# Optimization experiments

Hardware: AMD Instinct MI355X
Metric: run time of the kernel (lower is better)

## Reference

```python
import jax, jax.numpy as jnp
import numpy as np

N = 32            # batch (age.shape[0])
N_SAMPLE = 8
S = N * N_SAMPLE  # posterior samples
T = 1024          # len_param
K = 64            # len_window
D = 4             # dim_target
P = 8             # dim_param
LOG2PI = float(np.log(2.0 * np.pi))


def _windows(x, axis, num, size):
    # torch.unfold equivalent, but window axis inserted right after `axis`
    idx = jnp.arange(num)[:, None] + jnp.arange(size)[None, :]
    return jnp.take(x, idx, axis=axis)


def _coeffs(a_pad):
    # a_pad: (2K-2, D, 1) -> AR weight matrix d: (K, K, D)
    # d[t, k] = prod(a[t-K+1+k+1 .. t]) with trailing 1 (reversed cumprod of windows)
    b = _windows(a_pad, 0, K, K - 1)                              # (K, K-1, D, 1)
    c = jnp.flip(jnp.cumprod(jnp.flip(b, 1), axis=1), 1)
    d = jnp.concatenate([c, jnp.ones_like(c[:, :1])], axis=1)      # (K, K, D, 1)
    return d[..., 0]                                               # (K, K, D)


def _window_param(z, d):
    # z: (S, K, D, P); d: (K, K, D) -> param: (S, K, D, P)
    z_pad = jnp.pad(z, ((0, 0), (K - 1, 0), (0, 0), (0, 0)))
    zwin = _windows(z_pad, 1, K, K)                                # (S, K, K, D, P)
    return jnp.einsum('stkdp,tkd->stdp', zwin, d)


def _forward(m, s_raw, a_raw, noise, dim_idx):
    mm = m[:, dim_idx]                         # (T, D, P)
    s = jax.nn.softplus(s_raw[:, dim_idx])     # scale_transform
    a = jax.nn.sigmoid(a_raw[:, dim_idx])      # (T-1, D, 1)
    # ---- first window ----
    a_pad = jnp.pad(a[:K - 1], ((K - 1, 0), (0, 0), (0, 0)))       # (2K-2, D, 1)
    mean = (1.0 - a_pad[K - 2:]) * mm[:K]                          # (K, D, P)
    sw = s[:K]
    z = mean + sw * noise[:, :K]                                   # rsample
    lp = -jnp.log(sw) - 0.5 * LOG2PI - 0.5 * ((z - mean) / sw) ** 2
    param = _window_param(z, _coeffs(a_pad))
    params, lps = [param], [lp]
    # ---- subsequent windows (sequential carry via param[:, -1]) ----
    for l in range(K, T, K):
        r = min(l + K, T)
        aw = a[l - 1:r - 1]                                        # (K, D, 1)
        mean = (1.0 - aw) * mm[l:r]
        sw = s[l:r]
        z = mean + sw * noise[:, l:r]
        lp = -jnp.log(sw) - 0.5 * LOG2PI - 0.5 * ((z - mean) / sw) ** 2
        a_pad = jnp.pad(aw[1:], ((K - 1, 0), (0, 0), (0, 0)))
        p = _window_param(z, _coeffs(a_pad))
        p = p + jnp.cumprod(aw, axis=0)[None] * param[:, -1][:, None]
        params.append(p)
        lps.append(lp)
        param = p
    return jnp.concatenate(params, axis=1), jnp.concatenate(lps, axis=1)


def setup_inputs() -> dict:
    key = jax.random.key(0)
    k = jax.random.split(key, 6)
    return {
        'y': jax.random.normal(k[0], (1, T, D), dtype=jnp.float32),
        'age': jax.random.uniform(k[1], (N,), dtype=jnp.float32),
        'm': 0.1 * jax.random.normal(k[2], (T, D, P), dtype=jnp.float32),
        's_raw': 0.1 * jax.random.normal(k[3], (T, D, P), dtype=jnp.float32) - 6.0,
        'a_raw': jax.random.normal(k[4], (T - 1, D, 1), dtype=jnp.float32),
        'noise': jax.random.normal(k[5], (S, T, D, P), dtype=jnp.float32),
        'cond_sample': jnp.zeros((S, D, P), dtype=jnp.float32),
        'dim_idx': jnp.arange(D, dtype=jnp.int32),
        'compute_log_prob': 1,
    }


def reference(y, age, m, s_raw, a_raw, noise, cond_sample, dim_idx, compute_log_prob):
    param, log_prob = _forward(m, s_raw, a_raw, noise, dim_idx)
    if compute_log_prob:
        return (param, log_prob)
    return param
```

## Files before the change

### kernel.cpp

```cpp
#include <hip/hip_runtime.h>
#include <hip/hip_bf16.h>

#define T_DIM 1024
#define D_DIM 4
#define P_DIM 8
#define S_DIM 256
#define DP 32
#define TDP (T_DIM * DP)
#define LOG2PI_F 1.8378770664093453f

__global__ __launch_bounds__(256) void build_tbl(
    const float* __restrict__ m,
    const float* __restrict__ s_raw,
    const float* __restrict__ a_raw,
    const int* __restrict__ dim_idx,
    float4* __restrict__ tbl)
{
    int idx = blockIdx.x * 256 + threadIdx.x;
    int t  = idx >> 5;
    int dp = idx & 31;
    int d  = dp >> 3;
    int p  = dp & 7;
    int di = dim_idx[d];

    float mm = m[(t * D_DIM + di) * P_DIM + p];
    float sr = s_raw[(t * D_DIM + di) * P_DIM + p];
    float sv = (sr > 20.0f) ? sr : log1pf(expf(sr));

    float A = 0.0f;
    if (t > 0) {
        float ar = a_raw[(t - 1) * D_DIM + di];
        A = 1.0f / (1.0f + expf(-ar));
    }
    float mean = (1.0f - A) * mm;
    float nls  = -logf(sv) - 0.5f * LOG2PI_F;

    tbl[idx] = make_float4(mean, sv, nls, A);
}

__global__ __launch_bounds__(256) void scan_kernel(
    const float* __restrict__ noise,
    const float4* __restrict__ tbl,
    float* __restrict__ param_out,
    float* __restrict__ lp_out)
{
    const int s   = blockIdx.x;
    const int tid = threadIdx.x;
    const int dp  = tid & 31;
    const int cj  = tid >> 5;

    __shared__ float sh_pl[8][32];
    __shared__ float sh_m[8][32];
    __shared__ float sh_ci[8][32];

    const size_t sbase = (size_t)s * TDP;

    float carry = 0.0f;

    float  na[8];
    float4 ca[8];
    {
        const int tb = (cj * 8) * DP + dp;
        #pragma unroll
        for (int k = 0; k < 8; ++k) {
            na[k] = noise[sbase + tb + k * DP];
            ca[k] = tbl[tb + k * DP];
        }
    }

    for (int tile = 0; tile < 16; ++tile) {
        float  nb[8];
        float4 cb[8];
        {
            const int tn  = (tile + 1 < 16) ? tile + 1 : 0;
            const int tb2 = (tn * 64 + cj * 8) * DP + dp;
            #pragma unroll
            for (int k = 0; k < 8; ++k) {
                nb[k] = noise[sbase + tb2 + k * DP];
                cb[k] = tbl[tb2 + k * DP];
            }
        }

        const int tb = (tile * 64 + cj * 8) * DP + dp;

        float pl[8], Mk[8];
        float rp = 0.0f, rm = 1.0f;
        #pragma unroll
        for (int k = 0; k < 8; ++k) {
            const float n = na[k];
            const float z = ca[k].x + ca[k].y * n;
            lp_out[sbase + tb + k * DP] = ca[k].z - 0.5f * n * n;
            rp = z + ca[k].w * rp;
            rm = rm * ca[k].w;
            pl[k] = rp;
            Mk[k] = rm;
        }

        sh_pl[cj][dp] = rp;
        sh_m[cj][dp]  = rm;
        __syncthreads();

        if (cj == 0) {
            float cr = carry;
            #pragma unroll
            for (int cc = 0; cc < 8; ++cc) {
                sh_ci[cc][dp] = cr;
                cr = sh_pl[cc][dp] + sh_m[cc][dp] * cr;
            }
            carry = cr;
        }
        __syncthreads();

        const float ci = sh_ci[cj][dp];
        #pragma unroll
        for (int k = 0; k < 8; ++k) {
            param_out[sbase + tb + k * DP] = pl[k] + Mk[k] * ci;
        }

        #pragma unroll
        for (int k = 0; k < 8; ++k) { na[k] = nb[k]; ca[k] = cb[k]; }
    }
}

extern "C" void kernel_launch(void* const* d_in, const int* in_sizes, int n_in,
                              void* d_out, int out_size, void* d_ws, size_t ws_size,
                              hipStream_t stream)
{
    const float* m      = (const float*)d_in[2];
    const float* s_raw  = (const float*)d_in[3];
    const float* a_raw  = (const float*)d_in[4];
    const float* noise  = (const float*)d_in[5];
    const int*   dimidx = (const int*)d_in[7];

    float4* tbl = (float4*)d_ws;

    float* param_out = (float*)d_out;
    float* lp_out    = param_out + (size_t)S_DIM * TDP;

    build_tbl<<<TDP / 256, 256, 0, stream>>>(m, s_raw, a_raw, dimidx, tbl);
    scan_kernel<<<S_DIM, 256, 0, stream>>>(noise, tbl, param_out, lp_out);
}
```

Measured before the change: 126.1 us.

## Scan whole sequence per block with 1024 threads, wave shuffles and SoA table

The scan kernel now uses 1024 threads per sample. Each thread handles 8 timesteps of 4 contiguous dp lanes using float4 loads and stores, which replaces the 16 serial tiles of the old kernel. The coefficient table moves from array-of-float4 to structure-of-arrays so the accesses vectorise. The cross-chunk carry combines a wave-level shuffle scan with one 16-step shared-memory pass, which removes the per-tile barriers and serial carry loop. In exchange, register pressure rises with 1024-thread blocks, and the explicit next-tile prefetch of the old kernel is gone.

Measured after the change: 129.7 us. +2.8%, slower.

```diff
diff --git a/kernel.cpp b/kernel.cpp
--- a/kernel.cpp
+++ b/kernel.cpp
@@ -1,5 +1,4 @@
 #include <hip/hip_runtime.h>
-#include <hip/hip_bf16.h>
 
 #define T_DIM 1024
 #define D_DIM 4
@@ -14,111 +13,132 @@
     const float* __restrict__ s_raw,
     const float* __restrict__ a_raw,
     const int* __restrict__ dim_idx,
-    float4* __restrict__ tbl)
+    float* __restrict__ tbl)
 {
     int idx = blockIdx.x * 256 + threadIdx.x;
-    int t  = idx >> 5;
-    int dp = idx & 31;
-    int d  = dp >> 3;
-    int p  = dp & 7;
+    int t = idx >> 5, dp = idx & 31, d = dp >> 3, p = dp & 7;
     int di = dim_idx[d];
 
     float mm = m[(t * D_DIM + di) * P_DIM + p];
     float sr = s_raw[(t * D_DIM + di) * P_DIM + p];
     float sv = (sr > 20.0f) ? sr : log1pf(expf(sr));
+    float A = 0.0f;
+    if (t > 0) A = 1.0f / (1.0f + expf(-a_raw[(t - 1) * D_DIM + di]));
 
-    float A = 0.0f;
-    if (t > 0) {
-        float ar = a_raw[(t - 1) * D_DIM + di];
-        A = 1.0f / (1.0f + expf(-ar));
-    }
-    float mean = (1.0f - A) * mm;
-    float nls  = -logf(sv) - 0.5f * LOG2PI_F;
-
-    tbl[idx] = make_float4(mean, sv, nls, A);
+    tbl[idx]           = (1.0f - A) * mm;
+    tbl[TDP + idx]     = sv;
+    tbl[2 * TDP + idx] = -logf(sv) - 0.5f * LOG2PI_F;
+    tbl[3 * TDP + idx] = A;
 }
 
-__global__ __launch_bounds__(256) void scan_kernel(
+__global__ __launch_bounds__(1024) void scan_kernel(
     const float* __restrict__ noise,
-    const float4* __restrict__ tbl,
+    const float* __restrict__ tbl,
     float* __restrict__ param_out,
     float* __restrict__ lp_out)
 {
-    const int s   = blockIdx.x;
-    const int tid = threadIdx.x;
-    const int dp  = tid & 31;
-    const int cj  = tid >> 5;
+    const int tid  = threadIdx.x;
+    const int qc   = tid & 7;
+    const int cj   = tid >> 3;
+    const int cjw  = cj & 7;
+    const int wg   = tid >> 6;
 
-    __shared__ float sh_pl[8][32];
-    __shared__ float sh_m[8][32];
-    __shared__ float sh_ci[8][32];
+    __shared__ float wtp[16][32];
+    __shared__ float wtm[16][32];
+    __shared__ float wci[16][32];
 
-    const size_t sbase = (size_t)s * TDP;
+    const size_t sbase = (size_t)blockIdx.x * TDP;
+    const int    off0  = cj * 8 * DP + qc * 4;
 
-    float carry = 0.0f;
+    float4 pl[8], Mk[8];
+    float4 rp = make_float4(0.f, 0.f, 0.f, 0.f);
+    float4 rm = make_float4(1.f, 1.f, 1.f, 1.f);
+#pragma unroll
+    for (int k = 0; k < 8; ++k) {
+        const int o = off0 + k * DP;
+        const float4 n  = *(const float4*)(noise + sbase + o);
+        const float4 me = *(const float4*)(tbl + o);
+        const float4 sv = *(const float4*)(tbl + TDP + o);
+        const float4 nl = *(const float4*)(tbl + 2 * TDP + o);
+        const float4 Aa = *(const float4*)(tbl + 3 * TDP + o);
 
-    float  na[8];
-    float4 ca[8];
-    {
-        const int tb = (cj * 8) * DP + dp;
-        #pragma unroll
-        for (int k = 0; k < 8; ++k) {
-            na[k] = noise[sbase + tb + k * DP];
-            ca[k] = tbl[tb + k * DP];
+        float4 lp;
+        lp.x = nl.x - 0.5f * n.x * n.x;
+        lp.y = nl.y - 0.5f * n.y * n.y;
+        lp.z = nl.z - 0.5f * n.z * n.z;
+        lp.w = nl.w - 0.5f * n.w * n.w;
+        *(float4*)(lp_out + sbase + o) = lp;
+
+        float4 z;
+        z.x = me.x + sv.x * n.x;
+        z.y = me.y + sv.y * n.y;
+        z.z = me.z + sv.z * n.z;
+        z.w = me.w + sv.w * n.w;
+
+        rp.x = z.x + Aa.x * rp.x;  rm.x *= Aa.x;
+        rp.y = z.y + Aa.y * rp.y;  rm.y *= Aa.y;
+        rp.z = z.z + Aa.z * rp.z;  rm.z *= Aa.z;
+        rp.w = z.w + Aa.w * rp.w;  rm.w *= Aa.w;
+        pl[k] = rp;
+        Mk[k] = rm;
+    }
+
+#pragma unroll
+    for (int off = 1; off < 8; off <<= 1) {
+        const int d = off * 8;
+        float4 pp, pm;
+        pp.x = __shfl_up(rp.x, d, 64);  pm.x = __shfl_up(rm.x, d, 64);
+        pp.y = __shfl_up(rp.y, d, 64);  pm.y = __shfl_up(rm.y, d, 64);
+        pp.z = __shfl_up(rp.z, d, 64);  pm.z = __shfl_up(rm.z, d, 64);
+        pp.w = __shfl_up(rp.w, d, 64);  pm.w = __shfl_up(rm.w, d, 64);
+        if (cjw >= off) {
+            rp.x += rm.x * pp.x;  rm.x *= pm.x;
+            rp.y += rm.y * pp.y;  rm.y *= pm.y;
+            rp.z += rm.z * pp.z;  rm.z *= pm.z;
+            rp.w += rm.w * pp.w;  rm.w *= pm.w;
         }
     }
 
-    for (int tile = 0; tile < 16; ++tile) {
-        float  nb[8];
-        float4 cb[8];
-        {
-            const int tn  = (tile + 1 < 16) ? tile + 1 : 0;
-            const int tb2 = (tn * 64 + cj * 8) * DP + dp;
-            #pragma unroll
-            for (int k = 0; k < 8; ++k) {
-                nb[k] = noise[sbase + tb2 + k * DP];
-                cb[k] = tbl[tb2 + k * DP];
-            }
+    if (cjw == 7) {
+        *(float4*)&wtp[wg][qc * 4] = rp;
+        *(float4*)&wtm[wg][qc * 4] = rm;
+    }
+    __syncthreads();
+    if (tid < 32) {
+        float c = 0.0f;
+#pragma unroll
+        for (int g = 0; g < 16; ++g) {
+            wci[g][tid] = c;
+            c = wtp[g][tid] + wtm[g][tid] * c;
         }
+    }
+    __syncthreads();
 
-        const int tb = (tile * 64 + cj * 8) * DP + dp;
+    float4 ep, em;
+    ep.x = __shfl_up(rp.x, 8, 64);  em.x = __shfl_up(rm.x, 8, 64);
+    ep.y = __shfl_up(rp.y, 8, 64);  em.y = __shfl_up(rm.y, 8, 64);
+    ep.z = __shfl_up(rp.z, 8, 64);  em.z = __shfl_up(rm.z, 8, 64);
+    ep.w = __shfl_up(rp.w, 8, 64);  em.w = __shfl_up(rm.w, 8, 64);
+    if (cjw == 0) {
+        ep = make_float4(0.f, 0.f, 0.f, 0.f);
+        em = make_float4(1.f, 1.f, 1.f, 1.f);
+    }
+    const float4 ci = *(const float4*)&wci[wg][qc * 4];
+    float4 carry;
+    carry.x = ep.x + em.x * ci.x;
+    carry.y = ep.y + em.y * ci.y;
+    carry.z = ep.z + em.z * ci.z;
+    carry.w = ep.w + em.w * ci.w;
 
-        float pl[8], Mk[8];
-        float rp = 0.0f, rm = 1.0f;
-        #pragma unroll
-        for (int k = 0; k < 8; ++k) {
-            const float n = na[k];
-            const float z = ca[k].x + ca[k].y * n;
-            lp_out[sbase + tb + k * DP] = ca[k].z - 0.5f * n * n;
-            rp = z + ca[k].w * rp;
-            rm = rm * ca[k].w;
-            pl[k] = rp;
-            Mk[k] = rm;
-        }
-
-        sh_pl[cj][dp] = rp;
-        sh_m[cj][dp]  = rm;
-        __syncthreads();
-
-        if (cj == 0) {
-            float cr = carry;
-            #pragma unroll
-            for (int cc = 0; cc < 8; ++cc) {
-                sh_ci[cc][dp] = cr;
-                cr = sh_pl[cc][dp] + sh_m[cc][dp] * cr;
-            }
-            carry = cr;
-        }
-        __syncthreads();
-
-        const float ci = sh_ci[cj][dp];
-        #pragma unroll
-        for (int k = 0; k < 8; ++k) {
-            param_out[sbase + tb + k * DP] = pl[k] + Mk[k] * ci;
-        }
-
-        #pragma unroll
-        for (int k = 0; k < 8; ++k) { na[k] = nb[k]; ca[k] = cb[k]; }
+#pragma unroll
+    for (int k = 0; k < 8; ++k) {
+        const int o = off0 + k * DP;
+        float4 pv;
+        pv.x = pl[k].x + Mk[k].x * carry.x;
+        pv.y = pl[k].y + Mk[k].y * carry.y;
+        pv.z = pl[k].z + Mk[k].z * carry.z;
+        pv.w = pl[k].w + Mk[k].w * carry.w;
+        *(float4*)(param_out + sbase + o) = pv;
     }
 }
 
@@ -132,11 +152,11 @@
     const float* noise  = (const float*)d_in[5];
     const int*   dimidx = (const int*)d_in[7];
 
-    float4* tbl = (float4*)d_ws;
+    float* tbl = (float*)d_ws;
 
     float* param_out = (float*)d_out;
     float* lp_out    = param_out + (size_t)S_DIM * TDP;
 
     build_tbl<<<TDP / 256, 256, 0, stream>>>(m, s_raw, a_raw, dimidx, tbl);
-    scan_kernel<<<S_DIM, 256, 0, stream>>>(noise, tbl, param_out, lp_out);
+    scan_kernel<<<S_DIM, 1024, 0, stream>>>(noise, tbl, param_out, lp_out);
 }
```
